# Performance work log

Measured on AMD Instinct MI355X. Metric: run time of the kernel, lower is better.

Reference implementation:

```python
import jax, jax.numpy as jnp
import numpy as np

N_NODES = 100000

def setup_inputs() -> dict:
    key = jax.random.key(0)
    k1, k2, k3, k4, k5 = jax.random.split(key, 5)
    F_in, H, C = 128, 64, 40
    x = jax.random.normal(k1, (N_NODES, F_in), dtype=jnp.float32)
    edge_index = jax.random.randint(k2, (2, 1600000), 0, N_NODES, dtype=jnp.int64)
    # GCNConv weights (no bias), Glorot-ish scale
    W0 = jax.random.normal(k3, (F_in, H), dtype=jnp.float32) / np.sqrt(F_in)
    W1 = jax.random.normal(k4, (H, H), dtype=jnp.float32) / np.sqrt(H)
    W2 = jax.random.normal(k5, (H, C), dtype=jnp.float32) / np.sqrt(H)
    return {"x": x, "edge_index": edge_index, "W0": W0, "W1": W1, "W2": W2}


def _gcn_norm(edge_index, num_nodes):
    # Add self-loops, compute symmetric normalization D^-1/2 A D^-1/2
    loop = jnp.arange(num_nodes, dtype=edge_index.dtype)
    src = jnp.concatenate([edge_index[0], loop])
    dst = jnp.concatenate([edge_index[1], loop])
    deg = jax.ops.segment_sum(jnp.ones_like(dst, dtype=jnp.float32), dst,
                              num_segments=num_nodes)
    dinv = jnp.where(deg > 0, jax.lax.rsqrt(deg), 0.0)
    norm = dinv[src] * dinv[dst]  # [E + N]
    return src, dst, norm


def reference(x, edge_index, W0, W1, W2):
    N = x.shape[0]
    src, dst, norm = _gcn_norm(edge_index, N)

    def conv(h, W):
        h = h @ W                                   # [N, d_out]
        msg = h[src] * norm[:, None]                # gather + scale  [E+N, d_out]
        return jax.ops.segment_sum(msg, dst, num_segments=N)

    h = jax.nn.relu(conv(x, W0))
    h = jax.nn.relu(conv(h, W1))
    h = jax.nn.relu(conv(h, W2))
    return h
```

## Files before the change

kernel.cpp:

```cpp
#include <hip/hip_runtime.h>
#include <hip/hip_fp16.h>

#define N_FEAT0 128
#define HID 64
#define NCLS 40

#define BSH 9
#define BSZ 512
#define BCAP 12288
#define STILE 4096

__global__ __launch_bounds__(256) void scatter_kernel(const int* __restrict__ esrc,
                                                      const int* __restrict__ edst,
                                                      int* __restrict__ bfill,
                                                      int* __restrict__ slab, int E) {
  __shared__ int cnt[256];
  __shared__ int base[256];
  int t = threadIdx.x;
  int t0 = blockIdx.x * STILE;
  cnt[t] = 0;
  __syncthreads();

#pragma unroll 4
  for (int i = 0; i < STILE / 1024; ++i) {
    int e = t0 + i * 1024 + t * 4;
    if (e < E) {
      int4 d4 = *(const int4*)(edst + e);
      atomicAdd(&cnt[d4.x >> BSH], 1);
      atomicAdd(&cnt[d4.y >> BSH], 1);
      atomicAdd(&cnt[d4.z >> BSH], 1);
      atomicAdd(&cnt[d4.w >> BSH], 1);
    }
  }
  __syncthreads();
  int c = cnt[t];
  if (c > 0) base[t] = t * BCAP + atomicAdd(&bfill[t], c);
  cnt[t] = 0;
  __syncthreads();

#pragma unroll 4
  for (int i = 0; i < STILE / 1024; ++i) {
    int e = t0 + i * 1024 + t * 4;
    if (e < E) {
      int4 s4 = *(const int4*)(esrc + e);
      int4 d4 = *(const int4*)(edst + e);
#define EMIT(dd, ss)                                             \
      {                                                          \
        int b_ = (dd) >> BSH;                                    \
        int r_ = atomicAdd(&cnt[b_], 1);                         \
        slab[base[b_] + r_] = (((dd) & (BSZ - 1)) << 17) | (ss); \
      }
      EMIT(d4.x, s4.x)
      EMIT(d4.y, s4.y)
      EMIT(d4.z, s4.z)
      EMIT(d4.w, s4.w)
#undef EMIT
    }
  }
}

__global__ __launch_bounds__(512) void build_kernel(const int* __restrict__ slab,
                                                    const int* __restrict__ bfill,
                                                    int* __restrict__ row_ptr,
                                                    float* __restrict__ dinv,
                                                    int* __restrict__ ew,
                                                    int N, int nbuck) {
  __shared__ int cnt[512];
  __shared__ int pre[512];
  __shared__ int sc[256];
  int b = blockIdx.x;
  int t = threadIdx.x;
  int nbase = b << BSH;
  int nNodes = N - nbase;
  if (nNodes > BSZ) nNodes = BSZ;

  if (t < 256) sc[t] = (t < nbuck) ? bfill[t] : 0;
  __syncthreads();
  for (int off = 1; off < 256; off <<= 1) {
    int u = 0;
    if (t < 256 && t >= off) u = sc[t - off];
    __syncthreads();
    if (t < 256) sc[t] += u;
    __syncthreads();
  }
  int sz = bfill[b];
  int obase = sc[b] - sz;
  if (b == 0 && t == 0) row_ptr[N] = sc[255];
  cnt[t] = 0;
  __syncthreads();

  int sbeg = b * BCAP;

  for (int r = t; r < sz; r += 512) atomicAdd(&cnt[((unsigned)slab[sbeg + r]) >> 17], 1);
  __syncthreads();

  int c = cnt[t];
  pre[t] = c;
  __syncthreads();
  for (int off = 1; off < 512; off <<= 1) {
    int u = (t >= off) ? pre[t - off] : 0;
    __syncthreads();
    pre[t] += u;
    __syncthreads();
  }
  int ex = pre[t] - c;

  if (t < nNodes) {
    row_ptr[nbase + t] = obase + ex;
    dinv[nbase + t] = rsqrtf((float)(c + 1));
  }
  __syncthreads();
  pre[t] = ex;
  cnt[t] = 0;
  __syncthreads();

  for (int r = t; r < sz; r += 512) {
    int rec = slab[sbeg + r];
    int dloc = ((unsigned)rec) >> 17;
    int rank = atomicAdd(&cnt[dloc], 1);
    ew[obase + pre[dloc] + rank] = rec & 0x1FFFF;
  }
}

template <int K, int NC>
__global__ __launch_bounds__(256) void gemm_kernel(const float* __restrict__ A,
                                                   const float* __restrict__ W,
                                                   __half* __restrict__ Out,
                                                   const float* __restrict__ rowscale,
                                                   int N) {
  constexpr int BK = 64;
  constexpr int LDSS = 68;
  __shared__ float As[128 * LDSS];

  int t = threadIdx.x;
  int lane = t & 63;
  int wave = t >> 6;
  int c4 = lane & 15;
  int qr = lane >> 4;
  int r0 = blockIdx.x * 128;

  int wc = 4 * c4;
  if (wc > NC - 4) wc = NC - 4;
  bool cok = (wc == 4 * c4);

  float4 acc[8];
#pragma unroll
  for (int m = 0; m < 8; ++m) acc[m] = make_float4(0.f, 0.f, 0.f, 0.f);

  for (int kc = 0; kc < K; kc += BK) {
    __syncthreads();
#pragma unroll
    for (int i = 0; i < 8; ++i) {
      int idx = t + i * 256;
      int row = idx >> 4;
      int cq = idx & 15;
      int gr = r0 + row;
      if (gr >= N) gr = N - 1;
      float4 v = *(const float4*)(A + (size_t)gr * K + kc + 4 * cq);
      *(float4*)(As + row * LDSS + 4 * cq) = v;
    }
    __syncthreads();

#pragma unroll 2
    for (int kk = 0; kk < BK / 4; ++kk) {
      float4 w[4];
#pragma unroll
      for (int k = 0; k < 4; ++k)
        w[k] = *(const float4*)(W + (size_t)(kc + kk * 4 + k) * NC + wc);
#pragma unroll
      for (int m = 0; m < 8; ++m) {
        int lrow = wave * 32 + qr + 4 * m;
        float4 a = *(const float4*)(As + lrow * LDSS + kk * 4);
        acc[m].x = fmaf(a.x, w[0].x, acc[m].x);
        acc[m].y = fmaf(a.x, w[0].y, acc[m].y);
        acc[m].z = fmaf(a.x, w[0].z, acc[m].z);
        acc[m].w = fmaf(a.x, w[0].w, acc[m].w);
        acc[m].x = fmaf(a.y, w[1].x, acc[m].x);
        acc[m].y = fmaf(a.y, w[1].y, acc[m].y);
        acc[m].z = fmaf(a.y, w[1].z, acc[m].z);
        acc[m].w = fmaf(a.y, w[1].w, acc[m].w);
        acc[m].x = fmaf(a.z, w[2].x, acc[m].x);
        acc[m].y = fmaf(a.z, w[2].y, acc[m].y);
        acc[m].z = fmaf(a.z, w[2].z, acc[m].z);
        acc[m].w = fmaf(a.z, w[2].w, acc[m].w);
        acc[m].x = fmaf(a.w, w[3].x, acc[m].x);
        acc[m].y = fmaf(a.w, w[3].y, acc[m].y);
        acc[m].z = fmaf(a.w, w[3].z, acc[m].z);
        acc[m].w = fmaf(a.w, w[3].w, acc[m].w);
      }
    }
  }

  if (cok) {
#pragma unroll
    for (int m = 0; m < 8; ++m) {
      int gr = r0 + wave * 32 + qr + 4 * m;
      if (gr < N) {
        float ds = rowscale[gr];
        union { __half2 h[2]; uint2 u; } cv;
        cv.h[0] = __floats2half2_rn(ds * acc[m].x, ds * acc[m].y);
        cv.h[1] = __floats2half2_rn(ds * acc[m].z, ds * acc[m].w);
        *(uint2*)(Out + (size_t)gr * NC + wc) = cv.u;
      }
    }
  }
}

template <int NC>
__global__ __launch_bounds__(256) void gemm_h_kernel(const __half* __restrict__ A,
                                                     const float* __restrict__ W,
                                                     __half* __restrict__ Out,
                                                     const float* __restrict__ rowscale,
                                                     int N) {
  constexpr int K = 64;
  constexpr int LDSH = 76;
  __shared__ __half As[128 * LDSH];

  int t = threadIdx.x;
  int lane = t & 63;
  int wave = t >> 6;
  int c4 = lane & 15;
  int qr = lane >> 4;
  int r0 = blockIdx.x * 128;

  int wc = 4 * c4;
  if (wc > NC - 4) wc = NC - 4;
  bool cok = (wc == 4 * c4);

  float4 acc[8];
#pragma unroll
  for (int m = 0; m < 8; ++m) acc[m] = make_float4(0.f, 0.f, 0.f, 0.f);

#pragma unroll
  for (int i = 0; i < 4; ++i) {
    int idx = t + i * 256;
    int row = idx >> 3;
    int cq = idx & 7;
    int gr = r0 + row;
    if (gr >= N) gr = N - 1;
    uint4 v = *(const uint4*)(A + (size_t)gr * K + cq * 8);
    *(uint4*)(As + row * LDSH + cq * 8) = v;
  }
  __syncthreads();

#pragma unroll 2
  for (int kk = 0; kk < 8; ++kk) {
    float4 w[8];
#pragma unroll
    for (int k = 0; k < 8; ++k)
      w[k] = *(const float4*)(W + (size_t)(kk * 8 + k) * NC + wc);
#pragma unroll
    for (int m = 0; m < 8; ++m) {
      int lrow = wave * 32 + qr + 4 * m;
      uint4 av = *(const uint4*)(As + lrow * LDSH + kk * 8);
      const __half2* h2 = (const __half2*)&av;
      float2 f0 = __half22float2(h2[0]);
      float2 f1 = __half22float2(h2[1]);
      float2 f2 = __half22float2(h2[2]);
      float2 f3 = __half22float2(h2[3]);
#define FMA4(aa, ww)                              \
      acc[m].x = fmaf(aa, ww.x, acc[m].x);        \
      acc[m].y = fmaf(aa, ww.y, acc[m].y);        \
      acc[m].z = fmaf(aa, ww.z, acc[m].z);        \
      acc[m].w = fmaf(aa, ww.w, acc[m].w);
      FMA4(f0.x, w[0]) FMA4(f0.y, w[1])
      FMA4(f1.x, w[2]) FMA4(f1.y, w[3])
      FMA4(f2.x, w[4]) FMA4(f2.y, w[5])
      FMA4(f3.x, w[6]) FMA4(f3.y, w[7])
#undef FMA4
    }
  }

  if (cok) {
#pragma unroll
    for (int m = 0; m < 8; ++m) {
      int gr = r0 + wave * 32 + qr + 4 * m;
      if (gr < N) {
        float ds = rowscale[gr];
        union { __half2 h[2]; uint2 u; } cv;
        cv.h[0] = __floats2half2_rn(ds * acc[m].x, ds * acc[m].y);
        cv.h[1] = __floats2half2_rn(ds * acc[m].z, ds * acc[m].w);
        *(uint2*)(Out + (size_t)gr * NC + wc) = cv.u;
      }
    }
  }
}

template <int F, bool HOUT>
__global__ __launch_bounds__(256) void agg_kernel(const __half* __restrict__ G,
                                                  const int* __restrict__ row_ptr,
                                                  const int* __restrict__ ew,
                                                  const float* __restrict__ dinv,
                                                  void* __restrict__ HoutV, int N) {
  constexpr int FO = F / 8;
  int gid = blockIdx.x * blockDim.x + threadIdx.x;
  int v = gid >> 6;
  if (v >= N) return;
  int lane = threadIdx.x & 63;
  int eg = lane >> 3;
  int fo = lane & 7;
  bool fok = (fo < FO);
  int foc = fok ? fo : FO - 1;

  float acc[8];
#pragma unroll
  for (int i = 0; i < 8; ++i) acc[i] = 0.f;

#define GLD(s) (*(const uint4*)(G + (size_t)(s) * F + foc * 8))
  auto addrow = [&](uint4 q) {
    const __half2* h = (const __half2*)&q;
#pragma unroll
    for (int i = 0; i < 4; ++i) {
      float2 f = __half22float2(h[i]);
      acc[2 * i] += f.x;
      acc[2 * i + 1] += f.y;
    }
  };

  if (eg == 0) addrow(GLD(v));

  int beg = __builtin_amdgcn_readfirstlane(row_ptr[v]);
  int end = __builtin_amdgcn_readfirstlane(row_ptr[v + 1]);
  int j = beg;
  for (; j + 16 <= end; j += 16) {
    int s0 = ew[j + eg];
    int s1 = ew[j + 8 + eg];
    uint4 a = GLD(s0);
    uint4 b = GLD(s1);
    addrow(a);
    addrow(b);
  }
  if (j + 8 <= end) {
    addrow(GLD(ew[j + eg]));
    j += 8;
  }
  {
    int idx = j + eg;
    if (idx < end) addrow(GLD(ew[idx]));
  }
#undef GLD

#pragma unroll
  for (int m = 8; m <= 32; m <<= 1) {
#pragma unroll
    for (int i = 0; i < 8; ++i) acc[i] += __shfl_xor(acc[i], m);
  }

  if (fok) {
    float dv = dinv[v];
    if constexpr (HOUT) {
      __half* Hout = (__half*)HoutV;
      union { __half2 h2[4]; uint4 u; } cv;
      cv.h2[0] = __floats2half2_rn(fmaxf(dv * acc[0], 0.f), fmaxf(dv * acc[1], 0.f));
      cv.h2[1] = __floats2half2_rn(fmaxf(dv * acc[2], 0.f), fmaxf(dv * acc[3], 0.f));
      cv.h2[2] = __floats2half2_rn(fmaxf(dv * acc[4], 0.f), fmaxf(dv * acc[5], 0.f));
      cv.h2[3] = __floats2half2_rn(fmaxf(dv * acc[6], 0.f), fmaxf(dv * acc[7], 0.f));
      *(uint4*)(Hout + (size_t)v * F + fo * 8) = cv.u;
    } else {
      float* Hout = (float*)HoutV;
      float4 o0, o1;
      o0.x = fmaxf(dv * acc[0], 0.f);
      o0.y = fmaxf(dv * acc[1], 0.f);
      o0.z = fmaxf(dv * acc[2], 0.f);
      o0.w = fmaxf(dv * acc[3], 0.f);
      o1.x = fmaxf(dv * acc[4], 0.f);
      o1.y = fmaxf(dv * acc[5], 0.f);
      o1.z = fmaxf(dv * acc[6], 0.f);
      o1.w = fmaxf(dv * acc[7], 0.f);
      float4* outp = (float4*)(Hout + (size_t)v * F + fo * 8);
      outp[0] = o0;
      outp[1] = o1;
    }
  }
}

extern "C" void kernel_launch(void* const* d_in, const int* in_sizes, int n_in,
                              void* d_out, int out_size, void* d_ws, size_t ws_size,
                              hipStream_t stream) {
  const float* x  = (const float*)d_in[0];
  const int*   eg = (const int*)d_in[1];
  const float* W0 = (const float*)d_in[2];
  const float* W1 = (const float*)d_in[3];
  const float* W2 = (const float*)d_in[4];
  float* out = (float*)d_out;

  const int N = in_sizes[0] / N_FEAT0;
  const int E = in_sizes[1] / 2;
  const int* esrc = eg;
  const int* edst = eg + E;
  const int nbuck = (N + BSZ - 1) >> BSH;

  char* p = (char*)d_ws;
  auto alloc = [&](size_t bytes) {
    char* r = p;
    p += (bytes + 255) & ~(size_t)255;
    return r;
  };
  int*    bfill   = (int*)alloc(256 * 4);
  int*    row_ptr = (int*)alloc((size_t)(N + 1) * 4);
  float*  dinv    = (float*)alloc((size_t)N * 4);
  int*    ew      = (int*)alloc((size_t)E * 4);
  __half* bufG    = (__half*)alloc((size_t)N * HID * 2);
  __half* bufH    = (__half*)alloc((size_t)N * HID * 2);
  __half* bufG3   = (__half*)alloc((size_t)N * NCLS * 2);
  int* slab = (int*)bufH;

  hipMemsetAsync(bfill, 0, 256 * 4, stream);

  const int sblocks = (E + STILE - 1) / STILE;
  scatter_kernel<<<sblocks, 256, 0, stream>>>(esrc, edst, bfill, slab, E);
  build_kernel<<<nbuck, 512, 0, stream>>>(slab, bfill, row_ptr, dinv, ew, N, nbuck);

  const int gblocks = (N + 127) / 128;
  const int ablocks = (N + 3) / 4;
  gemm_kernel<128, 64><<<gblocks, 256, 0, stream>>>(x, W0, bufG, dinv, N);
  agg_kernel<64, true><<<ablocks, 256, 0, stream>>>(bufG, row_ptr, ew, dinv, bufH, N);
  gemm_h_kernel<64><<<gblocks, 256, 0, stream>>>(bufH, W1, bufG, dinv, N);
  agg_kernel<64, true><<<ablocks, 256, 0, stream>>>(bufG, row_ptr, ew, dinv, bufH, N);
  gemm_h_kernel<40><<<gblocks, 256, 0, stream>>>(bufH, W2, bufG3, dinv, N);
  agg_kernel<40, false><<<ablocks, 256, 0, stream>>>(bufG3, row_ptr, ew, dinv, out, N);
}
```

Baseline: 334.6 us.

## Replace FP32 FMA GEMMs with fp16 MFMA kernels using pre-transposed weights

The three dense transforms now use the 16x16x32 f16 MFMA matrix instruction, one wave per 16-row tile. A small prep kernel converts and transposes W0/W1/W2 to fp16 so B fragments load as contiguous half8 vectors. x is converted from fp32 to fp16 on the fly, which drops some input precision, and the LDS staging is removed. The per-element half stores in the epilogue are less vectorised than before, and the dinv float4 read at the last tile may read past N unless N is a multiple of 16.

```diff
diff --git a/kernel.cpp b/kernel.cpp
--- a/kernel.cpp
+++ b/kernel.cpp
@@ -9,6 +9,9 @@
 #define BSZ 512
 #define BCAP 12288
 #define STILE 4096
+
+typedef _Float16 half8 __attribute__((ext_vector_type(8)));
+typedef float f32x4 __attribute__((ext_vector_type(4)));
 
 __global__ __launch_bounds__(256) void scatter_kernel(const int* __restrict__ esrc,
                                                       const int* __restrict__ edst,
@@ -122,166 +125,81 @@
   }
 }
 
-template <int K, int NC>
-__global__ __launch_bounds__(256) void gemm_kernel(const float* __restrict__ A,
-                                                   const float* __restrict__ W,
-                                                   __half* __restrict__ Out,
-                                                   const float* __restrict__ rowscale,
-                                                   int N) {
-  constexpr int BK = 64;
-  constexpr int LDSS = 68;
-  __shared__ float As[128 * LDSS];
-
-  int t = threadIdx.x;
-  int lane = t & 63;
-  int wave = t >> 6;
-  int c4 = lane & 15;
-  int qr = lane >> 4;
-  int r0 = blockIdx.x * 128;
-
-  int wc = 4 * c4;
-  if (wc > NC - 4) wc = NC - 4;
-  bool cok = (wc == 4 * c4);
-
-  float4 acc[8];
-#pragma unroll
-  for (int m = 0; m < 8; ++m) acc[m] = make_float4(0.f, 0.f, 0.f, 0.f);
-
-  for (int kc = 0; kc < K; kc += BK) {
-    __syncthreads();
-#pragma unroll
-    for (int i = 0; i < 8; ++i) {
-      int idx = t + i * 256;
-      int row = idx >> 4;
-      int cq = idx & 15;
-      int gr = r0 + row;
-      if (gr >= N) gr = N - 1;
-      float4 v = *(const float4*)(A + (size_t)gr * K + kc + 4 * cq);
-      *(float4*)(As + row * LDSS + 4 * cq) = v;
-    }
-    __syncthreads();
-
-#pragma unroll 2
-    for (int kk = 0; kk < BK / 4; ++kk) {
-      float4 w[4];
-#pragma unroll
-      for (int k = 0; k < 4; ++k)
-        w[k] = *(const float4*)(W + (size_t)(kc + kk * 4 + k) * NC + wc);
-#pragma unroll
-      for (int m = 0; m < 8; ++m) {
-        int lrow = wave * 32 + qr + 4 * m;
-        float4 a = *(const float4*)(As + lrow * LDSS + kk * 4);
-        acc[m].x = fmaf(a.x, w[0].x, acc[m].x);
-        acc[m].y = fmaf(a.x, w[0].y, acc[m].y);
-        acc[m].z = fmaf(a.x, w[0].z, acc[m].z);
-        acc[m].w = fmaf(a.x, w[0].w, acc[m].w);
-        acc[m].x = fmaf(a.y, w[1].x, acc[m].x);
-        acc[m].y = fmaf(a.y, w[1].y, acc[m].y);
-        acc[m].z = fmaf(a.y, w[1].z, acc[m].z);
-        acc[m].w = fmaf(a.y, w[1].w, acc[m].w);
-        acc[m].x = fmaf(a.z, w[2].x, acc[m].x);
-        acc[m].y = fmaf(a.z, w[2].y, acc[m].y);
-        acc[m].z = fmaf(a.z, w[2].z, acc[m].z);
-        acc[m].w = fmaf(a.z, w[2].w, acc[m].w);
-        acc[m].x = fmaf(a.w, w[3].x, acc[m].x);
-        acc[m].y = fmaf(a.w, w[3].y, acc[m].y);
-        acc[m].z = fmaf(a.w, w[3].z, acc[m].z);
-        acc[m].w = fmaf(a.w, w[3].w, acc[m].w);
-      }
-    }
-  }
-
-  if (cok) {
-#pragma unroll
-    for (int m = 0; m < 8; ++m) {
-      int gr = r0 + wave * 32 + qr + 4 * m;
-      if (gr < N) {
-        float ds = rowscale[gr];
-        union { __half2 h[2]; uint2 u; } cv;
-        cv.h[0] = __floats2half2_rn(ds * acc[m].x, ds * acc[m].y);
-        cv.h[1] = __floats2half2_rn(ds * acc[m].z, ds * acc[m].w);
-        *(uint2*)(Out + (size_t)gr * NC + wc) = cv.u;
-      }
-    }
-  }
-}
-
-template <int NC>
-__global__ __launch_bounds__(256) void gemm_h_kernel(const __half* __restrict__ A,
-                                                     const float* __restrict__ W,
-                                                     __half* __restrict__ Out,
-                                                     const float* __restrict__ rowscale,
-                                                     int N) {
-  constexpr int K = 64;
-  constexpr int LDSH = 76;
-  __shared__ __half As[128 * LDSH];
-
-  int t = threadIdx.x;
-  int lane = t & 63;
-  int wave = t >> 6;
-  int c4 = lane & 15;
-  int qr = lane >> 4;
-  int r0 = blockIdx.x * 128;
-
-  int wc = 4 * c4;
-  if (wc > NC - 4) wc = NC - 4;
-  bool cok = (wc == 4 * c4);
-
-  float4 acc[8];
-#pragma unroll
-  for (int m = 0; m < 8; ++m) acc[m] = make_float4(0.f, 0.f, 0.f, 0.f);
-
-#pragma unroll
-  for (int i = 0; i < 4; ++i) {
-    int idx = t + i * 256;
-    int row = idx >> 3;
-    int cq = idx & 7;
-    int gr = r0 + row;
-    if (gr >= N) gr = N - 1;
-    uint4 v = *(const uint4*)(A + (size_t)gr * K + cq * 8);
-    *(uint4*)(As + row * LDSH + cq * 8) = v;
-  }
-  __syncthreads();
-
-#pragma unroll 2
-  for (int kk = 0; kk < 8; ++kk) {
-    float4 w[8];
-#pragma unroll
-    for (int k = 0; k < 8; ++k)
-      w[k] = *(const float4*)(W + (size_t)(kk * 8 + k) * NC + wc);
-#pragma unroll
-    for (int m = 0; m < 8; ++m) {
-      int lrow = wave * 32 + qr + 4 * m;
-      uint4 av = *(const uint4*)(As + lrow * LDSH + kk * 8);
-      const __half2* h2 = (const __half2*)&av;
-      float2 f0 = __half22float2(h2[0]);
-      float2 f1 = __half22float2(h2[1]);
-      float2 f2 = __half22float2(h2[2]);
-      float2 f3 = __half22float2(h2[3]);
-#define FMA4(aa, ww)                              \
-      acc[m].x = fmaf(aa, ww.x, acc[m].x);        \
-      acc[m].y = fmaf(aa, ww.y, acc[m].y);        \
-      acc[m].z = fmaf(aa, ww.z, acc[m].z);        \
-      acc[m].w = fmaf(aa, ww.w, acc[m].w);
-      FMA4(f0.x, w[0]) FMA4(f0.y, w[1])
-      FMA4(f1.x, w[2]) FMA4(f1.y, w[3])
-      FMA4(f2.x, w[4]) FMA4(f2.y, w[5])
-      FMA4(f3.x, w[6]) FMA4(f3.y, w[7])
-#undef FMA4
-    }
-  }
-
-  if (cok) {
-#pragma unroll
-    for (int m = 0; m < 8; ++m) {
-      int gr = r0 + wave * 32 + qr + 4 * m;
-      if (gr < N) {
-        float ds = rowscale[gr];
-        union { __half2 h[2]; uint2 u; } cv;
-        cv.h[0] = __floats2half2_rn(ds * acc[m].x, ds * acc[m].y);
-        cv.h[1] = __floats2half2_rn(ds * acc[m].z, ds * acc[m].w);
-        *(uint2*)(Out + (size_t)gr * NC + wc) = cv.u;
-      }
+__global__ __launch_bounds__(256) void prep_w_kernel(const float* __restrict__ W0,
+                                                     const float* __restrict__ W1,
+                                                     const float* __restrict__ W2,
+                                                     __half* __restrict__ Wt0,
+                                                     __half* __restrict__ Wt1,
+                                                     __half* __restrict__ Wt2) {
+  int id = blockIdx.x * 256 + threadIdx.x;
+  if (id < 8192) {
+    int c = id >> 7, k = id & 127;
+    Wt0[id] = __float2half_rn(W0[k * 64 + c]);
+  } else if (id < 8192 + 4096) {
+    int i = id - 8192;
+    int c = i >> 6, k = i & 63;
+    Wt1[i] = __float2half_rn(W1[k * 64 + c]);
+  } else if (id < 8192 + 4096 + 3072) {
+    int i = id - 8192 - 4096;
+    int c = i >> 6, k = i & 63;
+    Wt2[i] = (c < NCLS) ? __float2half_rn(W2[k * NCLS + c]) : __half(0.f);
+  }
+}
+
+template <int K, int NC, bool AF32>
+__global__ __launch_bounds__(256) void gemm_mfma(const void* __restrict__ Av,
+                                                 const __half* __restrict__ Wt,
+                                                 __half* __restrict__ Out,
+                                                 const float* __restrict__ dinv,
+                                                 int N) {
+  constexpr int NT = (NC + 15) / 16;
+  int lane = threadIdx.x & 63;
+  int r16 = lane & 15;
+  int kq = lane >> 4;
+  int wid = blockIdx.x * 4 + (threadIdx.x >> 6);
+  int ntiles = (N + 15) >> 4;
+  if (wid >= ntiles) return;
+  int r0 = wid << 4;
+
+  const __half* Ah = (const __half*)Av;
+  const float* Af = (const float*)Av;
+  int arow = r0 + r16;
+  if (arow >= N) arow = N - 1;
+
+  f32x4 acc[NT];
+#pragma unroll
+  for (int t2 = 0; t2 < NT; ++t2) acc[t2] = (f32x4){0.f, 0.f, 0.f, 0.f};
+
+#pragma unroll
+  for (int s = 0; s < K / 32; ++s) {
+    half8 a;
+    if constexpr (AF32) {
+      const float* ap = Af + (size_t)arow * K + s * 32 + kq * 8;
+      float4 v0 = *(const float4*)ap;
+      float4 v1 = *(const float4*)(ap + 4);
+      a[0] = (_Float16)v0.x; a[1] = (_Float16)v0.y;
+      a[2] = (_Float16)v0.z; a[3] = (_Float16)v0.w;
+      a[4] = (_Float16)v1.x; a[5] = (_Float16)v1.y;
+      a[6] = (_Float16)v1.z; a[7] = (_Float16)v1.w;
+    } else {
+      a = *(const half8*)(Ah + (size_t)arow * K + s * 32 + kq * 8);
+    }
+#pragma unroll
+    for (int t2 = 0; t2 < NT; ++t2) {
+      half8 b = *(const half8*)(Wt + (size_t)(t2 * 16 + r16) * K + s * 32 + kq * 8);
+      acc[t2] = __builtin_amdgcn_mfma_f32_16x16x32_f16(a, b, acc[t2], 0, 0, 0);
+    }
+  }
+
+  float4 dv = *(const float4*)(dinv + r0 + kq * 4);
+  float ds[4] = {dv.x, dv.y, dv.z, dv.w};
+#pragma unroll
+  for (int b = 0; b < 4; ++b) {
+    int gr = r0 + kq * 4 + b;
+#pragma unroll
+    for (int t2 = 0; t2 < NT; ++t2) {
+      int col = t2 * 16 + r16;
+      if (col < NC) Out[(size_t)gr * NC + col] = __float2half_rn(ds[b] * acc[t2][b]);
     }
   }
 }
@@ -400,6 +318,9 @@
   int*    row_ptr = (int*)alloc((size_t)(N + 1) * 4);
   float*  dinv    = (float*)alloc((size_t)N * 4);
   int*    ew      = (int*)alloc((size_t)E * 4);
+  __half* Wt0     = (__half*)alloc(8192 * 2);
+  __half* Wt1     = (__half*)alloc(4096 * 2);
+  __half* Wt2     = (__half*)alloc(3072 * 2);
   __half* bufG    = (__half*)alloc((size_t)N * HID * 2);
   __half* bufH    = (__half*)alloc((size_t)N * HID * 2);
   __half* bufG3   = (__half*)alloc((size_t)N * NCLS * 2);
@@ -407,16 +328,18 @@
 
   hipMemsetAsync(bfill, 0, 256 * 4, stream);
 
+  prep_w_kernel<<<60, 256, 0, stream>>>(W0, W1, W2, Wt0, Wt1, Wt2);
   const int sblocks = (E + STILE - 1) / STILE;
   scatter_kernel<<<sblocks, 256, 0, stream>>>(esrc, edst, bfill, slab, E);
   build_kernel<<<nbuck, 512, 0, stream>>>(slab, bfill, row_ptr, dinv, ew, N, nbuck);
 
-  const int gblocks = (N + 127) / 128;
+  const int ntiles = (N + 15) / 16;
+  const int mblocks = (ntiles + 3) / 4;
   const int ablocks = (N + 3) / 4;
-  gemm_kernel<128, 64><<<gblocks, 256, 0, stream>>>(x, W0, bufG, dinv, N);
+  gemm_mfma<128, 64, true><<<mblocks, 256, 0, stream>>>(x, Wt0, bufG, dinv, N);
   agg_kernel<64, true><<<ablocks, 256, 0, stream>>>(bufG, row_ptr, ew, dinv, bufH, N);
-  gemm_h_kernel<64><<<gblocks, 256, 0, stream>>>(bufH, W1, bufG, dinv, N);
+  gemm_mfma<64, 64, false><<<mblocks, 256, 0, stream>>>(bufH, Wt1, bufG, dinv, N);
   agg_kernel<64, true><<<ablocks, 256, 0, stream>>>(bufG, row_ptr, ew, dinv, bufH, N);
-  gemm_h_kernel<40><<<gblocks, 256, 0, stream>>>(bufH, W2, bufG3, dinv, N);
+  gemm_mfma<64, 40, false><<<mblocks, 256, 0, stream>>>(bufH, Wt2, bufG3, dinv, N);
   agg_kernel<40, false><<<ablocks, 256, 0, stream>>>(bufG3, row_ptr, ew, dinv, out, N);
 }
```

New measurement: 303.8 us. 1.1x faster.
